# Performance work log

Measured on AMD Instinct MI355X. Metric: run time of the kernel, lower is better.

The kernel has to match this reference:

```python
import jax, jax.numpy as jnp
import numpy as np

B, CIN, HW = 32, 64, 56
K, KS, STRIDE, PAD = 128, 3, 1, 1


def setup_inputs() -> dict:
    key = jax.random.key(0)
    kx, kw, kb = jax.random.split(key, 3)
    x = jax.random.normal(kx, (B, CIN, HW, HW), dtype=jnp.float32)
    weight = jax.random.normal(kw, (K, CIN, KS, KS), dtype=jnp.float32)
    offset = jax.random.normal(kb, (K, 1, 1), dtype=jnp.float32)
    return {"x": x, "weight": weight, "offset": offset}


def reference(x, weight, offset):
    # conv2d (NCHW, OIHW) with stride/padding, then add per-kernel scalar offset.
    # Equivalent to the module's im2col (create_window_column_matrix) + matmul
    # + reshape, plus self.offset broadcast over (B, K, s, s).
    out = jax.lax.conv_general_dilated(
        x, weight,
        window_strides=(STRIDE, STRIDE),
        padding=[(PAD, PAD), (PAD, PAD)],
        dimension_numbers=("NCHW", "OIHW", "NCHW"),
    )
    return out + offset  # offset (K,1,1) broadcasts against (B,K,s,s)
```

## Files before the change

### kernel.cpp

```cpp
#include <hip/hip_runtime.h>
#include <hip/hip_bf16.h>

namespace {

using frag_t    = __attribute__((ext_vector_type(8))) short;
using f32x4     = __attribute__((ext_vector_type(4))) float;
using float4_t  = __attribute__((ext_vector_type(4))) float;

constexpr int BATCH = 32;
constexpr int CIN   = 64;
constexpr int HWD   = 56;
constexpr int KOUT  = 128;
constexpr int SP    = HWD * HWD;
constexpr int KD    = 9 * CIN;
constexpr int BN    = 64;
constexpr int HALO  = 57;
constexpr int WINR  = BN + 2 * HALO;
constexpr int NSTA  = 192;
constexpr int NT    = SP / BN;
constexpr int NWG   = NT * BATCH;
constexpr int TT    = BATCH * (SP / 64);
constexpr int WB2   = (KOUT * KD) / 256;
constexpr int KHSTR = 18 * 2048;

__device__ inline unsigned short f2bf(float f) {
    __hip_bfloat16 h = __float2bfloat16(f);
    return __builtin_bit_cast(unsigned short, h);
}

__global__ __launch_bounds__(256)
void prep_kernel(const float* __restrict__ x, const float* __restrict__ w,
                 unsigned short* __restrict__ wpA2, unsigned short* __restrict__ xT)
{
    if (blockIdx.x >= TT) {
        const int idx = (blockIdx.x - TT) * 256 + threadIdx.x;
        const int q   = idx & 7;
        int r1 = idx >> 3;
        const int l  = r1 & 63;  r1 >>= 6;
        const int mi = r1 & 3;   r1 >>= 2;
        const int kc = r1 % 18;
        const int kh = r1 / 18;
        const int kout = kh * 64 + mi * 16 + (l & 15);
        const int kk   = kc * 32 + (l >> 4) * 8 + q;
        const int c = kk & 63, t = kk >> 6, ky = t / 3, kx = t - ky * 3;
        wpA2[idx] = f2bf(w[((kout * CIN + c) * 3 + ky) * 3 + kx]);
        return;
    }
    __shared__ float ls[64][68];
    const int bb   = blockIdx.x / (SP / 64);
    const int tile = blockIdx.x - bb * (SP / 64);
    const int sp0  = tile * 64;
    const int tid  = threadIdx.x;
    const int cq   = tid >> 4;
    const int spo  = (tid & 15) * 4;
    const float* xb = x + (size_t)bb * CIN * SP;
    #pragma unroll
    for (int j = 0; j < 4; ++j) {
        const int c = cq + 16 * j;
        float4_t v = *(const float4_t*)&xb[(size_t)c * SP + sp0 + spo];
        ls[spo + 0][c] = v.x; ls[spo + 1][c] = v.y;
        ls[spo + 2][c] = v.z; ls[spo + 3][c] = v.w;
    }
    __syncthreads();
    unsigned short* xo = xT + (size_t)(bb * SP + sp0) * 64;
    #pragma unroll
    for (int j = 0; j < 2; ++j) {
        const int s  = tid + 256 * j;
        const int sp = s >> 3, e = s & 7;
        frag_t u;
        #pragma unroll
        for (int q = 0; q < 8; ++q)
            u[q] = (short)f2bf(ls[sp][e * 8 + q]);
        *(frag_t*)&xo[sp * 64 + e * 8] = u;
    }
}

__global__ __launch_bounds__(256, 4)
void conv_b2(const unsigned short* __restrict__ xT, const unsigned short* __restrict__ wpA2,
             const float* __restrict__ off, float* __restrict__ out)
{
    __shared__ unsigned short xs[NSTA * 64];

    const int d    = blockIdx.x;
    const int wk   = (d & 7) * (NWG / 8) + (d >> 3);
    const int b    = wk / NT;
    const int sp0  = (wk - b * NT) * BN;
    const int tid  = threadIdx.x;
    const int lane = tid & 63;
    const int wid  = tid >> 6;

    {
        const unsigned short* xb = xT + (size_t)b * SP * 64;
        const int lsw = ((lane & 7) * 8) ^ ((lane >> 3) << 3);
        #pragma unroll
        for (int it = 0; it < 6; ++it) {
            const int R0 = it * 32 + wid * 8;
            const int r  = R0 + (lane >> 3);
            if (r < WINR) {
                int g = sp0 - HALO + r;
                g = min(max(g, 0), SP - 1);
                __builtin_amdgcn_global_load_lds(
                    (const __attribute__((address_space(1))) unsigned int*)
                        (xb + (size_t)g * 64 + lsw),
                    (__attribute__((address_space(3))) unsigned int*)
                        &xs[R0 * 64 + lane * 8],
                    16, 0, 0);
            }
        }
        *(unsigned int*)&xs[184 * 64 + tid * 2] = 0u;
    }
    asm volatile("s_waitcnt vmcnt(0)" ::: "memory");
    __syncthreads();

    const int l15 = lane & 15;
    const int l4  = lane >> 4;
    const int cread = 8 * l4;
    const int zaddr = 184 * 64 + cread;

    unsigned long long mbits = 0ull;
    int yv[4], xv[4];
    #pragma unroll
    for (int nf = 0; nf < 4; ++nf) {
        const int sp = sp0 + nf * 16 + l15;
        yv[nf] = sp / HWD;
        xv[nf] = sp - yv[nf] * HWD;
    }
    #pragma unroll
    for (int t = 0; t < 9; ++t) {
        const int dy = t / 3 - 1, dx = t % 3 - 1;
        #pragma unroll
        for (int nf = 0; nf < 4; ++nf) {
            const bool v = ((unsigned)(yv[nf] + dy) < (unsigned)HWD) &
                           ((unsigned)(xv[nf] + dx) < (unsigned)HWD);
            mbits |= (unsigned long long)(v ? 1 : 0) << (t * 4 + nf);
        }
    }

    const unsigned short* ap = wpA2 + (size_t)(wid >> 1) * KHSTR
                                    + (wid & 1) * 1024 + lane * 8;
    const frag_t zf = {0,0,0,0,0,0,0,0};
    f32x4 acc[2][4] = {};

    #pragma unroll
    for (int p = 0; p < 6; ++p) {
        frag_t aB[6];
        #pragma unroll
        for (int j = 0; j < 3; ++j)
            #pragma unroll
            for (int m = 0; m < 2; ++m)
                aB[j * 2 + m] = *(const frag_t*)(ap + (size_t)(p * 3 + j) * 2048 + m * 512);
        #pragma unroll
        for (int j = 0; j < 3; ++j) {
            const int kc = p * 3 + j;
            const int t  = kc >> 1;
            const int c0 = (kc & 1) * 32;
            const int shift = (t / 3 - 1) * HWD + (t % 3 - 1);
            const int row0b = l15 + HALO + shift;
            const int sw    = (row0b & 7) << 3;
            const int cadr  = (c0 + cread) ^ sw;
            const unsigned m4 = (unsigned)((mbits >> (t * 4)) & 15ull);
            frag_t bfr[4];
            #pragma unroll
            for (int nf = 0; nf < 4; ++nf) {
                const int ba = (row0b + 16 * nf) * 64 + cadr;
                const int ra = ((m4 >> nf) & 1u) ? ba : zaddr;
                bfr[nf] = *(const frag_t*)&xs[ra];
            }
            #pragma unroll
            for (int m = 0; m < 2; ++m)
                #pragma unroll
                for (int nf = 0; nf < 4; ++nf)
                    acc[m][nf] = __builtin_amdgcn_mfma_f32_16x16x32_bf16(
                        aB[j * 2 + m], bfr[nf], acc[m][nf], 0, 0, 0);
        }
    }

    const int spn = sp0 + l15;
    #pragma unroll
    for (int m = 0; m < 2; ++m) {
        const int km = wid * 32 + m * 16 + 4 * l4;
        #pragma unroll
        for (int reg = 0; reg < 4; ++reg) {
            const int  kk  = km + reg;
            const float ofv = off[kk];
            float* ob = out + (size_t)(b * KOUT + kk) * SP;
            #pragma unroll
            for (int nf = 0; nf < 4; ++nf)
                ob[spn + 16 * nf] = acc[m][nf][reg] + ofv;
        }
    }
}

__global__ __launch_bounds__(256)
void conv3x3_kernel(const float* __restrict__ x, const float* __restrict__ w,
                    const float* __restrict__ off, float* __restrict__ out)
{
    const int s  = blockIdx.x * 256 + threadIdx.x;
    const int b  = s / SP;
    const int sp = s - b * SP;
    const int y  = sp / HWD;
    const int xx = sp - y * HWD;
    const int k0 = blockIdx.y * 4;

    const int   xm1 = (xx > 0) ? xx - 1 : 0;
    const int   xp1 = (xx < HWD - 1) ? xx + 1 : HWD - 1;
    const float m0  = (xx > 0) ? 1.f : 0.f;
    const float m2  = (xx < HWD - 1) ? 1.f : 0.f;

    int ro[3]; float msk[3][3];
    #pragma unroll
    for (int ky = 0; ky < 3; ++ky) {
        const int  yy = y + ky - 1;
        const bool ok = (unsigned)yy < (unsigned)HWD;
        const float rm = ok ? 1.f : 0.f;
        ro[ky] = (ok ? yy : 0) * HWD;
        msk[ky][0] = rm * m0; msk[ky][1] = rm; msk[ky][2] = rm * m2;
    }
    float acc[4] = {0.f, 0.f, 0.f, 0.f};
    const float* xb = x + (size_t)b * CIN * SP;
    for (int c = 0; c < CIN; ++c) {
        const float* xc = xb + (size_t)c * SP;
        #pragma unroll
        for (int ky = 0; ky < 3; ++ky) {
            const float* xr = xc + ro[ky];
            const float v0 = xr[xm1] * msk[ky][0];
            const float v1 = xr[xx]  * msk[ky][1];
            const float v2 = xr[xp1] * msk[ky][2];
            const int wi = c * 9 + ky * 3;
            #pragma unroll
            for (int kk = 0; kk < 4; ++kk) {
                const float* wr = w + (size_t)(k0 + kk) * (CIN * 9) + wi;
                acc[kk] = fmaf(v0, wr[0], acc[kk]);
                acc[kk] = fmaf(v1, wr[1], acc[kk]);
                acc[kk] = fmaf(v2, wr[2], acc[kk]);
            }
        }
    }
    #pragma unroll
    for (int kk = 0; kk < 4; ++kk)
        out[(size_t)(b * KOUT + k0 + kk) * SP + sp] = acc[kk] + off[k0 + kk];
}

}

extern "C" void kernel_launch(void* const* d_in, const int* in_sizes, int n_in,
                              void* d_out, int out_size, void* d_ws, size_t ws_size,
                              hipStream_t stream)
{
    const float* x   = (const float*)d_in[0];
    const float* w   = (const float*)d_in[1];
    const float* off = (const float*)d_in[2];
    float* out = (float*)d_out;

    const size_t wpa_bytes = (size_t)KOUT * KD * 2;
    const size_t xt_bytes  = (size_t)BATCH * SP * CIN * 2;

    if (ws_size >= wpa_bytes + xt_bytes) {
        unsigned short* wpA2 = (unsigned short*)d_ws;
        unsigned short* xT   = (unsigned short*)((char*)d_ws + wpa_bytes);
        prep_kernel<<<TT + WB2, 256, 0, stream>>>(x, w, wpA2, xT);
        conv_b2<<<NWG, dim3(256, 1, 1), 0, stream>>>(xT, wpA2, off, out);
    } else {
        dim3 grid((BATCH * SP) / 256, KOUT / 4);
        conv3x3_kernel<<<grid, dim3(256, 1, 1), 0, stream>>>(x, w, off, out);
    }
}
```

Before: 40.13 us.

## Widen conv tile to 128 spatial positions per workgroup

Doubles the spatial tile each workgroup computes from 64 to 128 positions. Each weight fragment loaded from global memory now feeds twice as many MFMAs, and the halo overhead of the staged input window shrinks relative to the useful rows. The price is twice the accumulator registers, a larger LDS window, and lower occupancy (launch bounds drop from 4 to 3). The tile count no longer divides the spatial size, so a guard on output stores handles the partial last tile.

```diff
diff --git a/kernel.cpp b/kernel.cpp
--- a/kernel.cpp
+++ b/kernel.cpp
@@ -13,11 +13,11 @@
 constexpr int KOUT  = 128;
 constexpr int SP    = HWD * HWD;
 constexpr int KD    = 9 * CIN;
-constexpr int BN    = 64;
+constexpr int BN    = 128;
 constexpr int HALO  = 57;
 constexpr int WINR  = BN + 2 * HALO;
-constexpr int NSTA  = 192;
-constexpr int NT    = SP / BN;
+constexpr int NSTA  = 248;
+constexpr int NT    = SP / BN + 1;
 constexpr int NWG   = NT * BATCH;
 constexpr int TT    = BATCH * (SP / 64);
 constexpr int WB2   = (KOUT * KD) / 256;
@@ -75,9 +75,9 @@
     }
 }
 
-__global__ __launch_bounds__(256, 4)
-void conv_b2(const unsigned short* __restrict__ xT, const unsigned short* __restrict__ wpA2,
-             const float* __restrict__ off, float* __restrict__ out)
+__global__ __launch_bounds__(256, 3)
+void conv_wide(const unsigned short* __restrict__ xT, const unsigned short* __restrict__ wpA2,
+               const float* __restrict__ off, float* __restrict__ out)
 {
     __shared__ unsigned short xs[NSTA * 64];
 
@@ -93,7 +93,7 @@
         const unsigned short* xb = xT + (size_t)b * SP * 64;
         const int lsw = ((lane & 7) * 8) ^ ((lane >> 3) << 3);
         #pragma unroll
-        for (int it = 0; it < 6; ++it) {
+        for (int it = 0; it < 8; ++it) {
             const int R0 = it * 32 + wid * 8;
             const int r  = R0 + (lane >> 3);
             if (r < WINR) {
@@ -107,7 +107,8 @@
                     16, 0, 0);
             }
         }
-        *(unsigned int*)&xs[184 * 64 + tid * 2] = 0u;
+        if (tid < 192)
+            *(unsigned int*)&xs[242 * 64 + tid * 2] = 0u;
     }
     asm volatile("s_waitcnt vmcnt(0)" ::: "memory");
     __syncthreads();
@@ -115,31 +116,34 @@
     const int l15 = lane & 15;
     const int l4  = lane >> 4;
     const int cread = 8 * l4;
-    const int zaddr = 184 * 64 + cread;
-
-    unsigned long long mbits = 0ull;
-    int yv[4], xv[4];
-    #pragma unroll
-    for (int nf = 0; nf < 4; ++nf) {
-        const int sp = sp0 + nf * 16 + l15;
-        yv[nf] = sp / HWD;
-        xv[nf] = sp - yv[nf] * HWD;
-    }
-    #pragma unroll
-    for (int t = 0; t < 9; ++t) {
-        const int dy = t / 3 - 1, dx = t % 3 - 1;
-        #pragma unroll
-        for (int nf = 0; nf < 4; ++nf) {
-            const bool v = ((unsigned)(yv[nf] + dy) < (unsigned)HWD) &
-                           ((unsigned)(xv[nf] + dx) < (unsigned)HWD);
-            mbits |= (unsigned long long)(v ? 1 : 0) << (t * 4 + nf);
+    const int zaddr = 242 * 64 + cread;
+
+    unsigned tm[9];
+    {
+        int yv[8], xv[8];
+        #pragma unroll
+        for (int nf = 0; nf < 8; ++nf) {
+            const int sp = sp0 + nf * 16 + l15;
+            yv[nf] = sp / HWD;
+            xv[nf] = sp - yv[nf] * HWD;
+        }
+        #pragma unroll
+        for (int t = 0; t < 9; ++t) {
+            const int dy = t / 3 - 1, dx = t % 3 - 1;
+            unsigned m = 0;
+            #pragma unroll
+            for (int nf = 0; nf < 8; ++nf) {
+                const bool v = ((unsigned)(yv[nf] + dy) < (unsigned)HWD) &
+                               ((unsigned)(xv[nf] + dx) < (unsigned)HWD);
+                m |= (v ? 1u : 0u) << nf;
+            }
+            tm[t] = m;
         }
     }
 
     const unsigned short* ap = wpA2 + (size_t)(wid >> 1) * KHSTR
                                     + (wid & 1) * 1024 + lane * 8;
-    const frag_t zf = {0,0,0,0,0,0,0,0};
-    f32x4 acc[2][4] = {};
+    f32x4 acc[2][8] = {};
 
     #pragma unroll
     for (int p = 0; p < 6; ++p) {
@@ -158,20 +162,24 @@
             const int row0b = l15 + HALO + shift;
             const int sw    = (row0b & 7) << 3;
             const int cadr  = (c0 + cread) ^ sw;
-            const unsigned m4 = (unsigned)((mbits >> (t * 4)) & 15ull);
-            frag_t bfr[4];
-            #pragma unroll
-            for (int nf = 0; nf < 4; ++nf) {
-                const int ba = (row0b + 16 * nf) * 64 + cadr;
-                const int ra = ((m4 >> nf) & 1u) ? ba : zaddr;
-                bfr[nf] = *(const frag_t*)&xs[ra];
-            }
-            #pragma unroll
-            for (int m = 0; m < 2; ++m)
+            const unsigned m8 = tm[t];
+            #pragma unroll
+            for (int h = 0; h < 2; ++h) {
+                frag_t bfr[4];
                 #pragma unroll
-                for (int nf = 0; nf < 4; ++nf)
-                    acc[m][nf] = __builtin_amdgcn_mfma_f32_16x16x32_bf16(
-                        aB[j * 2 + m], bfr[nf], acc[m][nf], 0, 0, 0);
+                for (int q = 0; q < 4; ++q) {
+                    const int nf = h * 4 + q;
+                    const int ba = (row0b + 16 * nf) * 64 + cadr;
+                    const int ra = ((m8 >> nf) & 1u) ? ba : zaddr;
+                    bfr[q] = *(const frag_t*)&xs[ra];
+                }
+                #pragma unroll
+                for (int m = 0; m < 2; ++m)
+                    #pragma unroll
+                    for (int q = 0; q < 4; ++q)
+                        acc[m][h * 4 + q] = __builtin_amdgcn_mfma_f32_16x16x32_bf16(
+                            aB[j * 2 + m], bfr[q], acc[m][h * 4 + q], 0, 0, 0);
+            }
         }
     }
 
@@ -185,8 +193,10 @@
             const float ofv = off[kk];
             float* ob = out + (size_t)(b * KOUT + kk) * SP;
             #pragma unroll
-            for (int nf = 0; nf < 4; ++nf)
-                ob[spn + 16 * nf] = acc[m][nf][reg] + ofv;
+            for (int nf = 0; nf < 8; ++nf) {
+                const int sp = spn + 16 * nf;
+                if (sp < SP) ob[sp] = acc[m][nf][reg] + ofv;
+            }
         }
     }
 }
@@ -259,7 +269,7 @@
         unsigned short* wpA2 = (unsigned short*)d_ws;
         unsigned short* xT   = (unsigned short*)((char*)d_ws + wpa_bytes);
         prep_kernel<<<TT + WB2, 256, 0, stream>>>(x, w, wpA2, xT);
-        conv_b2<<<NWG, dim3(256, 1, 1), 0, stream>>>(xT, wpA2, off, out);
+        conv_wide<<<NWG, dim3(256, 1, 1), 0, stream>>>(xT, wpA2, off, out);
     } else {
         dim3 grid((BATCH * SP) / 256, KOUT / 4);
         conv3x3_kernel<<<grid, dim3(256, 1, 1), 0, stream>>>(x, w, off, out);
```

New measurement: 47.03 us. 17.2% more time.
